# Performance work log

Hardware: AMD Instinct MI355X
Metric: run time of the kernel (lower is better)

The kernel has to match this reference:

```python
import math
import jax, jax.numpy as jnp
import numpy as np

BN_EPS = 1e-5

def _lrelu(x, s):
    return jnp.where(x >= 0, x, s * x)

def _bn(x, g, b):
    # BatchNorm2d in train mode (torch default): biased batch stats over (B,H,W)
    mu = jnp.mean(x, axis=(0, 2, 3), keepdims=True)
    var = jnp.mean((x - mu) ** 2, axis=(0, 2, 3), keepdims=True)
    return (x - mu) / jnp.sqrt(var + BN_EPS) * g[None, :, None, None] + b[None, :, None, None]

def _knn(x, x2, k):
    # x: [B,d,P], x2: [B,d,S] -> idx [B,k,S]: k nearest points of x for each column of x2
    inner = -2.0 * jnp.einsum('bdp,bds->bps', x, x2)
    xx = jnp.sum(x ** 2, axis=1)[:, :, None]    # [B,P,1]
    xx2 = jnp.sum(x2 ** 2, axis=1)[:, None, :]  # [B,1,S]
    d = -xx - inner - xx2                        # [B,P,S], larger = closer
    _, idx = jax.lax.top_k(jnp.transpose(d, (0, 2, 1)), k)  # [B,S,k]
    return jnp.transpose(idx, (0, 2, 1))         # [B,k,S]

def _gather_nb(X, idx, s, k):
    # faithful to torch gether_neibour, including its flat-reshape layout
    B, C, P = X.shape
    base = jnp.arange(B)[:, None, None] * P
    flat = (idx + base).reshape(-1)
    Xt = jnp.transpose(X, (0, 2, 1)).reshape(B * P, C)
    return Xt[flat].reshape(B, s, k, C)

def _c2d(x, W, b):
    return jnp.einsum('oc,bcpk->bopk', W, x) + b[None, :, None, None]

def _c1d(x, W, b):
    return jnp.einsum('oc,bcp->bop', W, x) + b[None, :, None]

def _forward(x, W_pos, b_pos, g2, be2, W_conv, b_conv, g1, be1, W_a1, b_a1, W_a2, b_a2, W_b1, b_b1, W_b2, b_b2, num_points):
    B, C, P = x.shape
    k = 8
    s = num_points
    # ---- Dynamic_sampling_M: uniform mesh over (x,y) bbox, snap to nearest event ----
    L = int(math.ceil(math.sqrt(s)))
    m = jnp.arange(L, dtype=x.dtype) / L
    m01 = jnp.tile(m[None, :], (L, 1)).reshape(1, 1, L * L)
    m02 = jnp.tile(m[:, None], (1, L)).reshape(1, 1, L * L)
    mesh = jnp.broadcast_to(jnp.concatenate([m01, m02], axis=1), (B, 2, L * L))
    Px = jax.lax.stop_gradient(x[:, :2, :])  # knn runs under torch.no_grad
    mn = Px.min(axis=2, keepdims=True)
    mx = Px.max(axis=2, keepdims=True)
    PS = mesh * (mx - mn) + mn
    idx0 = _knn(Px, PS, 1)                                   # [B,1,L*L]
    sp = _gather_nb(x, idx0, L * L, 1)[:, :, 0, :].transpose(0, 2, 1)  # [B,C,s]
    idx = _knn(jax.lax.stop_gradient(x[:, :3, :]), jax.lax.stop_gradient(sp[:, :3, :]), k)  # [B,k,s]
    x1 = jnp.transpose(_gather_nb(x, idx, s, k), (0, 3, 1, 2))  # [B,C,s,k]
    # ---- positional encoding ----
    PA = x1[:, :3, :, :]
    PC = x1[:, :3, :, 0:1]
    diff = PA - PC
    sq = jnp.sum(diff ** 2, axis=1, keepdims=True)
    temp = jnp.where(sq > 0, jnp.sqrt(jnp.where(sq > 0, sq, 1.0)), 0.0)
    PEmb = jnp.concatenate([PA, jnp.broadcast_to(PC, PA.shape), diff, temp], axis=1)  # [B,10,s,k]
    PEmb = _lrelu(_bn(_c2d(PEmb, W_pos, b_pos), g2, be2), 0.2)
    x_ = _lrelu(_bn(_c2d(x1[:, :4, :, :], W_conv, b_conv), g1, be1), 0.2)
    feat = jnp.concatenate([x_, PEmb], axis=1)  # [B,64,s,k]
    att = _c2d(_lrelu(_c2d(feat, W_a1, b_a1), 0.2), W_a2, b_a2)  # [B,1,s,k]
    att = jax.nn.softmax(att, axis=-1)
    feat = jnp.sum(feat * att, axis=-1)  # [B,64,s]
    Fea1 = _c1d(feat, W_b1, b_b1)
    Fea2 = _c1d(x1[:, :4, :, 0], W_b2, b_b2)
    out = _lrelu(Fea1 + Fea2, 0.01)
    return jnp.concatenate([x1[:, :5, :, 0], out], axis=1)  # [B,69,s]

def setup_inputs() -> dict:
    key = jax.random.key(0)
    ks = jax.random.split(key, 8)
    B, C, P = 2, 5, 16384
    num_points = 4096  # perfect square required by the mesh sampler
    outc, inc, h = 64, 4, 32
    w = lambda k_, shape: jax.random.normal(k_, shape, jnp.float32) * 0.05
    x = jax.random.normal(ks[0], (B, C, P), jnp.float32)
    return dict(
        x=x,
        W_pos=w(ks[1], (h, 10)), b_pos=jnp.zeros((h,), jnp.float32),
        g2=jnp.ones((h,), jnp.float32), be2=jnp.zeros((h,), jnp.float32),
        W_conv=w(ks[2], (h, inc)), b_conv=jnp.zeros((h,), jnp.float32),
        g1=jnp.ones((h,), jnp.float32), be1=jnp.zeros((h,), jnp.float32),
        W_a1=w(ks[3], (32, outc)), b_a1=jnp.zeros((32,), jnp.float32),
        W_a2=w(ks[4], (1, 32)), b_a2=jnp.zeros((1,), jnp.float32),
        W_b1=w(ks[5], (outc, outc)), b_b1=jnp.zeros((outc,), jnp.float32),
        W_b2=w(ks[6], (outc, inc)), b_b2=jnp.zeros((outc,), jnp.float32),
        num_points=num_points,
    )

def reference(x, W_pos, b_pos, g2, be2, W_conv, b_conv, g1, be1, W_a1, b_a1, W_a2, b_a2, W_b1, b_b1, W_b2, b_b2, num_points):
    return _forward(x, W_pos, b_pos, g2, be2, W_conv, b_conv, g1, be1, W_a1, b_a1, W_a2, b_a2, W_b1, b_b1, W_b2, b_b2, num_points)
```

## Files before the change

kernel.cpp:

```cpp
#include <hip/hip_runtime.h>
#include <math.h>

#define B_ 2
#define P_ 16384
#define C_ 5
#define S_ 4096
#define KNN_ 8
#define L_ 64

typedef unsigned short u16;
typedef unsigned int u32;

__device__ int   g_idxk[B_ * KNN_ * S_];
__device__ float g_partials[256 * 128];

__device__ __forceinline__ float bf2f(u16 u) {
  union { u32 i; float f; } c; c.i = ((u32)u) << 16; return c.f;
}
__device__ __forceinline__ u16 f2bf(float f) {
  union { float f; u32 i; } c; c.f = f;
  u32 r = c.i + 0x7fffu + ((c.i >> 16) & 1u);
  return (u16)(r >> 16);
}
__device__ __forceinline__ float ldany(const void* p, int i, int f32) {
  return f32 ? ((const float*)p)[i] : bf2f(((const u16*)p)[i]);
}

__device__ __forceinline__ int keyidx(double w) {
  return 16383 - (int)(((u32)__double2loint(w) >> 6) & 16383u);
}
__device__ __forceinline__ void cmpswap(double& a, double& b) {
  double hi = fmax(a, b), lo = fmin(a, b);
  a = hi; b = lo;
}
__device__ __forceinline__ void flush8(double* a, double* k) {
  cmpswap(k[0], k[1]); cmpswap(k[2], k[3]); cmpswap(k[4], k[5]); cmpswap(k[6], k[7]);
  cmpswap(k[0], k[2]); cmpswap(k[1], k[3]); cmpswap(k[4], k[6]); cmpswap(k[5], k[7]);
  cmpswap(k[1], k[2]); cmpswap(k[5], k[6]);
  cmpswap(k[0], k[4]); cmpswap(k[1], k[5]); cmpswap(k[2], k[6]); cmpswap(k[3], k[7]);
  cmpswap(k[2], k[4]); cmpswap(k[3], k[5]);
  cmpswap(k[1], k[2]); cmpswap(k[3], k[4]); cmpswap(k[5], k[6]);
  a[0] = fmax(a[0], k[7]); a[1] = fmax(a[1], k[6]);
  a[2] = fmax(a[2], k[5]); a[3] = fmax(a[3], k[4]);
  a[4] = fmax(a[4], k[3]); a[5] = fmax(a[5], k[2]);
  a[6] = fmax(a[6], k[1]); a[7] = fmax(a[7], k[0]);
  cmpswap(a[0], a[4]); cmpswap(a[1], a[5]); cmpswap(a[2], a[6]); cmpswap(a[3], a[7]);
  cmpswap(a[0], a[2]); cmpswap(a[1], a[3]); cmpswap(a[4], a[6]); cmpswap(a[5], a[7]);
  cmpswap(a[0], a[1]); cmpswap(a[2], a[3]); cmpswap(a[4], a[5]); cmpswap(a[6], a[7]);
}

__device__ __forceinline__ int chk_bad(const void* p, int n, int tid) {
  int bad = 0;
  for (int i = tid; i < n; i += 256) {
    float f = bf2f(((const u16*)p)[i]);
    if (!(f == f) || fabsf(f) > 1024.0f) bad = 1;
  }
  return bad;
}

__global__ __launch_bounds__(256, 6) void k_knn(const void* __restrict__ xv) {
  __shared__ float4 s4[1024];
  __shared__ int sidx[4];
  __shared__ int sbad;
  __shared__ float sred[16];
  int tid = threadIdx.x;
  int l = tid & 63, g = tid >> 6;
  int sq = blockIdx.x * 4 + g;
  int b = sq >> 12;
  int s = sq & (S_ - 1);
  int base0 = b * C_ * P_, base1 = base0 + P_, base2 = base1 + P_;

  if (tid == 0) sbad = 0;
  __syncthreads();
  if (chk_bad(xv, 1024, tid)) atomicOr(&sbad, 1);
  __syncthreads();
  const int f32 = sbad;

  float mn0 = INFINITY, mx0 = -INFINITY, mn1 = INFINITY, mx1 = -INFINITY;
  for (int p = tid; p < P_; p += 256) {
    float v0 = ldany(xv, base0 + p, f32);
    float v1 = ldany(xv, base1 + p, f32);
    mn0 = fminf(mn0, v0); mx0 = fmaxf(mx0, v0);
    mn1 = fminf(mn1, v1); mx1 = fmaxf(mx1, v1);
  }
  for (int off = 32; off; off >>= 1) {
    mn0 = fminf(mn0, __shfl_down(mn0, off)); mx0 = fmaxf(mx0, __shfl_down(mx0, off));
    mn1 = fminf(mn1, __shfl_down(mn1, off)); mx1 = fmaxf(mx1, __shfl_down(mx1, off));
  }
  if (l == 0) {
    sred[g * 4 + 0] = mn0; sred[g * 4 + 1] = mx0;
    sred[g * 4 + 2] = mn1; sred[g * 4 + 3] = mx1;
  }
  __syncthreads();
  mn0 = fminf(fminf(sred[0], sred[4]), fminf(sred[8], sred[12]));
  mx0 = fmaxf(fmaxf(sred[1], sred[5]), fmaxf(sred[9], sred[13]));
  mn1 = fminf(fminf(sred[2], sred[6]), fminf(sred[10], sred[14]));
  mx1 = fmaxf(fmaxf(sred[3], sred[7]), fmaxf(sred[11], sred[15]));

  float mm0 = (float)(s & (L_ - 1)) * 0.015625f;
  float mm1 = (float)(s >> 6) * 0.015625f;
  float ps0 = __fadd_rn(__fmul_rn(mm0, __fsub_rn(mx0, mn0)), mn0);
  float ps1 = __fadd_rn(__fmul_rn(mm1, __fsub_rn(mx1, mn1)), mn1);
  float xx2 = __fadd_rn(__fmul_rn(ps0, ps0), __fmul_rn(ps1, ps1));
  float best = -INFINITY; int bestp = 0x7fffffff;
  for (int c = 0; c < 16; ++c) {
    __syncthreads();
#pragma unroll
    for (int r = 0; r < 4; ++r) {
      int i = r * 256 + tid;
      int gi = c * 1024 + i;
      float a0 = ldany(xv, base0 + gi, f32);
      float a1 = ldany(xv, base1 + gi, f32);
      float xx = __fadd_rn(__fmul_rn(a0, a0), __fmul_rn(a1, a1));
      s4[i] = make_float4(a0, a1, xx, 0.0f);
    }
    __syncthreads();
    for (int t = 0; t < 16; ++t) {
      float4 v = s4[t * 64 + l];
      int ix = c * 1024 + t * 64 + l;
      float dot = __fadd_rn(__fmul_rn(v.x, ps0), __fmul_rn(v.y, ps1));
      float inner = __fmul_rn(-2.0f, dot);
      float d = __fsub_rn(__fsub_rn(-v.z, inner), xx2);
      bool gt = d > best;
      best = gt ? d : best;
      bestp = gt ? ix : bestp;
    }
  }
  {
    float v = best; int ix = bestp;
    for (int m = 1; m < 64; m <<= 1) {
      float ov = __shfl_xor(v, m, 64); int op = __shfl_xor(ix, m, 64);
      if (ov > v || (ov == v && op < ix)) { v = ov; ix = op; }
    }
    if (l == 0) sidx[g] = ix;
  }
  __syncthreads();

  int qi = sidx[g] & (P_ - 1);
  float q0 = ldany(xv, base0 + qi, f32);
  float q1 = ldany(xv, base1 + qi, f32);
  float q2 = ldany(xv, base2 + qi, f32);
  float xx3q = __fadd_rn(__fadd_rn(__fmul_rn(q0, q0), __fmul_rn(q1, q1)),
                         __fmul_rn(q2, q2));
  double acc[8], kb[8];
#pragma unroll
  for (int k = 0; k < 8; ++k) acc[k] = -1.0;
  for (int c = 0; c < 16; ++c) {
    __syncthreads();
#pragma unroll
    for (int r = 0; r < 4; ++r) {
      int i = r * 256 + tid;
      int gi = c * 1024 + i;
      float a0 = ldany(xv, base0 + gi, f32);
      float a1 = ldany(xv, base1 + gi, f32);
      float a2 = ldany(xv, base2 + gi, f32);
      float xx = __fadd_rn(__fadd_rn(__fmul_rn(a0, a0), __fmul_rn(a1, a1)), __fmul_rn(a2, a2));
      s4[i] = make_float4(a0, a1, a2, xx);
    }
    __syncthreads();
#pragma unroll
    for (int t = 0; t < 16; ++t) {
      float4 v = s4[t * 64 + l];
      int ix = c * 1024 + t * 64 + l;
      u32 lob = ((u32)(16383 - ix)) << 6;
      float dot = __fadd_rn(__fadd_rn(__fmul_rn(v.x, q0), __fmul_rn(v.y, q1)),
                            __fmul_rn(v.z, q2));
      float inner = __fmul_rn(-2.0f, dot);
      float d = __fsub_rn(__fsub_rn(-v.w, inner), xx3q);
      u32 bits = __float_as_uint(d);
      u32 key = bits ^ ((u32)(((int)bits) >> 31) | 0x80000000u);
      kb[t & 7] = __hiloint2double((int)(0x3FF00000u | (key >> 12)),
                                   (int)((key << 20) | lob));
      if ((t & 7) == 7) flush8(acc, kb);
    }
  }
  double wk = 0.0;
#pragma unroll
  for (int r = 0; r < 8; ++r) {
    double w = acc[0];
    for (int m = 1; m < 64; m <<= 1) w = fmax(w, __shfl_xor(w, m, 64));
    if (l == r) wk = w;
    bool cns = (acc[0] == w);
#pragma unroll
    for (int k = 0; k < 7; ++k) acc[k] = cns ? acc[k + 1] : acc[k];
    acc[7] = cns ? -1.0 : acc[7];
  }
  if (l < 8) g_idxk[b * 32768 + l * 4096 + s] = keyidx(wk);
}

__global__ __launch_bounds__(256) void k_tail(const void* __restrict__ x,
                                              const void* __restrict__ Wpos,
                                              const void* __restrict__ bpos,
                                              const void* __restrict__ Wconv,
                                              const void* __restrict__ bconv) {
  __shared__ float sWpos[320], sbpos[32], sWconv[128], sbconv[32];
  __shared__ float sacc[16][128];
  __shared__ int sbx, sbw;
  int tid = threadIdx.x;
  if (tid == 0) { sbx = 0; sbw = 0; }
  __syncthreads();
  if (chk_bad(x, 1024, tid)) atomicOr(&sbx, 1);
  if (chk_bad(Wpos, 320, tid) | chk_bad(Wconv, 128, tid)) atomicOr(&sbw, 1);
  __syncthreads();
  const int f32 = sbx, wf32 = sbw;

  int id = blockIdx.x * 256 + tid;
  int b = id >> 15, n = id & 32767;
  const int* fb = g_idxk + b * 32768;
  int base0 = b * C_ * P_;
  int p = fb[n] & (P_ - 1);
  int p0 = fb[n & ~7] & (P_ - 1);
  float xvv[4], pc3[3];
#pragma unroll
  for (int cc = 0; cc < 4; ++cc) xvv[cc] = ldany(x, base0 + cc * P_ + p, f32);
#pragma unroll
  for (int cc = 0; cc < 3; ++cc) pc3[cc] = ldany(x, base0 + cc * P_ + p0, f32);

  for (int i2 = tid; i2 < 320; i2 += 256) sWpos[i2] = ldany(Wpos, i2, wf32);
  if (tid < 128) sWconv[tid] = ldany(Wconv, tid, wf32);
  if (tid < 32) { sbpos[tid] = ldany(bpos, tid, wf32); sbconv[tid] = ldany(bconv, tid, wf32); }
  __syncthreads();

  float d0 = xvv[0] - pc3[0], d1 = xvv[1] - pc3[1], d2 = xvv[2] - pc3[2];
  float sq = d0 * d0 + d1 * d1 + d2 * d2;
  float temp = (sq > 0.0f) ? sqrtf(sq) : 0.0f;
  float pe[10] = {xvv[0], xvv[1], xvv[2], pc3[0], pc3[1], pc3[2], d0, d1, d2, temp};
#pragma unroll
  for (int o = 0; o < 64; ++o) {
    float v;
    if (o < 32) {
      v = sbconv[o];
#pragma unroll
      for (int cc = 0; cc < 4; ++cc) v = fmaf(sWconv[o * 4 + cc], xvv[cc], v);
    } else {
      v = sbpos[o - 32];
#pragma unroll
      for (int cc = 0; cc < 10; ++cc) v = fmaf(sWpos[(o - 32) * 10 + cc], pe[cc], v);
    }
    float sv = v, qv = v * v;
    for (int m = 1; m < 16; m <<= 1) { sv += __shfl_xor(sv, m, 16); qv += __shfl_xor(qv, m, 16); }
    if ((tid & 15) == 0) { sacc[tid >> 4][o * 2] = sv; sacc[tid >> 4][o * 2 + 1] = qv; }
  }
  __syncthreads();
  if (tid < 128) {
    float a = 0.f;
#pragma unroll
    for (int w = 0; w < 16; ++w) a += sacc[w][tid];
    g_partials[blockIdx.x * 128 + tid] = a;
  }
}

__global__ __launch_bounds__(256) void k_pass2(const void* __restrict__ x,
                                               const void* __restrict__ Wpos,
                                               const void* __restrict__ bpos,
                                               const void* __restrict__ Wconv,
                                               const void* __restrict__ bconv,
                                               const void* __restrict__ g1,
                                               const void* __restrict__ be1,
                                               const void* __restrict__ g2,
                                               const void* __restrict__ be2,
                                               const void* __restrict__ Wa1,
                                               const void* __restrict__ ba1,
                                               const void* __restrict__ Wa2,
                                               const void* __restrict__ ba2,
                                               const void* __restrict__ Wb1,
                                               const void* __restrict__ bb1,
                                               const void* __restrict__ Wb2,
                                               const void* __restrict__ bb2,
                                               void* __restrict__ out) {
  __shared__ float sWpos[320], sbpos[32], sWconv[128], sbconv[32];
  __shared__ float sWa1[2048], sba1[32], sWa2[32];
  __shared__ float sWb1[64 * 65];
  __shared__ float sbb1[64], sWb2[256], sbb2[64], sstats[128];
  __shared__ float sp2[2][128];
  __shared__ float sba2;
  __shared__ int sbx, sbw;
  int tid = threadIdx.x;
  if (tid == 0) { sbx = 0; sbw = 0; }
  __syncthreads();
  if (chk_bad(x, 1024, tid)) atomicOr(&sbx, 1);
  if (chk_bad(Wa1, 2048, tid) | chk_bad(Wb1, 4096, tid)) atomicOr(&sbw, 1);
  __syncthreads();
  int xf32 = sbx, wf32 = sbw;

  int g = blockIdx.x * 32 + (tid >> 3);
  int j = tid & 7;
  int b = g >> 12, i = g & (S_ - 1);
  int n = i * 8 + j;
  const int* fb = g_idxk + b * 32768;
  int xbase = b * C_ * P_;
  int p = fb[n] & (P_ - 1);
  int p0 = fb[n & ~7] & (P_ - 1);
  float xvv[4];
#pragma unroll
  for (int c = 0; c < 4; ++c) xvv[c] = ldany(x, xbase + c * P_ + p, xf32);
  float pc3[3];
#pragma unroll
  for (int c = 0; c < 3; ++c) pc3[c] = ldany(x, xbase + c * P_ + p0, xf32);
  float xc0 = ldany(x, xbase + p0, xf32);
  float xc1 = ldany(x, xbase + P_ + p0, xf32);
  float xc2 = ldany(x, xbase + 2 * P_ + p0, xf32);
  float xc3 = ldany(x, xbase + 3 * P_ + p0, xf32);

  {
    int slot = tid & 127, half = tid >> 7;
    float a0 = 0.f, a1 = 0.f;
    for (int blk = half * 128; blk < half * 128 + 128; blk += 2) {
      a0 += g_partials[blk * 128 + slot];
      a1 += g_partials[(blk + 1) * 128 + slot];
    }
    sp2[half][slot] = a0 + a1;
  }
  for (int i2 = tid; i2 < 320; i2 += 256) sWpos[i2] = ldany(Wpos, i2, wf32);
  if (tid < 128) sWconv[tid] = ldany(Wconv, tid, wf32);
  if (tid < 32) { sbpos[tid] = ldany(bpos, tid, wf32); sbconv[tid] = ldany(bconv, tid, wf32); }
  for (int i2 = tid; i2 < 2048; i2 += 256) sWa1[i2] = ldany(Wa1, i2, wf32);
  for (int i2 = tid; i2 < 4096; i2 += 256) sWb1[(i2 >> 6) * 65 + (i2 & 63)] = ldany(Wb1, i2, wf32);
  if (tid >= 32 && tid < 64) { sba1[tid - 32] = ldany(ba1, tid - 32, wf32); sWa2[tid - 32] = ldany(Wa2, tid - 32, wf32); }
  if (tid >= 64 && tid < 128) { sbb1[tid - 64] = ldany(bb1, tid - 64, wf32); sbb2[tid - 64] = ldany(bb2, tid - 64, wf32); }
  sWb2[tid] = ldany(Wb2, tid, wf32);
  if (tid == 0) sba2 = ldany(ba2, 0, wf32);
  __syncthreads();
  if (tid >= 128 && tid < 192) {
    int ch = tid - 128;
    float sum = sp2[0][ch * 2] + sp2[1][ch * 2];
    float sq = sp2[0][ch * 2 + 1] + sp2[1][ch * 2 + 1];
    float mean = sum * (1.0f / 65536.0f);
    float var = sq * (1.0f / 65536.0f) - mean * mean;
    int o = ch & 31;
    float gg = ldany(ch < 32 ? g1 : g2, o, wf32);
    float be = ldany(ch < 32 ? be1 : be2, o, wf32);
    float scale = gg / sqrtf(var + 1e-5f);
    sstats[ch * 2] = scale;
    sstats[ch * 2 + 1] = be - mean * scale;
  }
  __syncthreads();

  float d0 = xvv[0] - pc3[0], d1 = xvv[1] - pc3[1], d2 = xvv[2] - pc3[2];
  float sq = d0 * d0 + d1 * d1 + d2 * d2;
  float temp = (sq > 0.0f) ? sqrtf(sq) : 0.0f;
  float pe[10] = {xvv[0], xvv[1], xvv[2], pc3[0], pc3[1], pc3[2], d0, d1, d2, temp};
  float feat[64];
#pragma unroll
  for (int o = 0; o < 32; ++o) {
    float acc = sbconv[o];
#pragma unroll
    for (int c = 0; c < 4; ++c) acc = fmaf(sWconv[o * 4 + c], xvv[c], acc);
    feat[o] = acc;
  }
#pragma unroll
  for (int o = 0; o < 32; ++o) {
    float acc = sbpos[o];
#pragma unroll
    for (int c = 0; c < 10; ++c) acc = fmaf(sWpos[o * 10 + c], pe[c], acc);
    feat[32 + o] = acc;
  }
#pragma unroll
  for (int c = 0; c < 64; ++c) {
    float v = fmaf(feat[c], sstats[c * 2], sstats[c * 2 + 1]);
    feat[c] = (v >= 0.f) ? v : 0.2f * v;
  }
  float att = sba2;
#pragma unroll 4
  for (int h = 0; h < 32; ++h) {
    float a0 = 0.f, a1 = 0.f, a2 = 0.f, a3 = 0.f;
#pragma unroll
    for (int c = 0; c < 64; c += 4) {
      a0 = fmaf(sWa1[h * 64 + c],     feat[c],     a0);
      a1 = fmaf(sWa1[h * 64 + c + 1], feat[c + 1], a1);
      a2 = fmaf(sWa1[h * 64 + c + 2], feat[c + 2], a2);
      a3 = fmaf(sWa1[h * 64 + c + 3], feat[c + 3], a3);
    }
    float acc = sba1[h] + ((a0 + a1) + (a2 + a3));
    acc = (acc >= 0.f) ? acc : 0.2f * acc;
    att = fmaf(sWa2[h], acc, att);
  }
  float mxv = att;
  for (int mk = 1; mk < 8; mk <<= 1) mxv = fmaxf(mxv, __shfl_xor(mxv, mk, 8));
  float e = expf(att - mxv);
  float se = e;
  for (int mk = 1; mk < 8; mk <<= 1) se += __shfl_xor(se, mk, 8);
  float a = e / se;
#pragma unroll
  for (int c = 0; c < 64; ++c) {
    float w = feat[c] * a;
    w += __shfl_xor(w, 1, 8);
    w += __shfl_xor(w, 2, 8);
    w += __shfl_xor(w, 4, 8);
    feat[c] = w;
  }
  int obase = b * 69 * S_;
#pragma unroll
  for (int oc = 0; oc < 8; ++oc) {
    int o = j * 8 + oc;
    float a0 = sbb1[o], a1 = 0.f, a2 = 0.f, a3 = 0.f;
#pragma unroll
    for (int c = 0; c < 64; c += 4) {
      a0 = fmaf(sWb1[o * 65 + c],     feat[c],     a0);
      a1 = fmaf(sWb1[o * 65 + c + 1], feat[c + 1], a1);
      a2 = fmaf(sWb1[o * 65 + c + 2], feat[c + 2], a2);
      a3 = fmaf(sWb1[o * 65 + c + 3], feat[c + 3], a3);
    }
    float acc = (a0 + a1) + (a2 + a3);
    float acc2 = sbb2[o];
    acc2 = fmaf(sWb2[o * 4 + 0], xc0, acc2);
    acc2 = fmaf(sWb2[o * 4 + 1], xc1, acc2);
    acc2 = fmaf(sWb2[o * 4 + 2], xc2, acc2);
    acc2 = fmaf(sWb2[o * 4 + 3], xc3, acc2);
    float r = acc + acc2;
    r = (r >= 0.f) ? r : 0.01f * r;
    int oi = obase + (5 + o) * S_ + i;
    if (xf32) ((float*)out)[oi] = r; else ((u16*)out)[oi] = f2bf(r);
  }
  if (j == 0) {
#pragma unroll
    for (int c = 0; c < 5; ++c) {
      int oi = obase + c * S_ + i;
      if (xf32) ((float*)out)[oi] = ((const float*)x)[xbase + c * P_ + p0];
      else      ((u16*)out)[oi]   = ((const u16*)x)[xbase + c * P_ + p0];
    }
  }
}

extern "C" void kernel_launch(void* const* d_in, const int* in_sizes, int n_in,
                              void* d_out, int out_size, void* d_ws, size_t ws_size,
                              hipStream_t stream) {
  const void* x     = d_in[0];
  const void* Wpos  = d_in[1];
  const void* bpos  = d_in[2];
  const void* g2    = d_in[3];
  const void* be2   = d_in[4];
  const void* Wconv = d_in[5];
  const void* bconv = d_in[6];
  const void* g1    = d_in[7];
  const void* be1   = d_in[8];
  const void* Wa1   = d_in[9];
  const void* ba1   = d_in[10];
  const void* Wa2   = d_in[11];
  const void* ba2   = d_in[12];
  const void* Wb1   = d_in[13];
  const void* bb1   = d_in[14];
  const void* Wb2   = d_in[15];
  const void* bb2   = d_in[16];
  (void)d_ws; (void)ws_size; (void)in_sizes; (void)n_in;

  hipLaunchKernelGGL(k_knn, dim3(2048), dim3(256), 0, stream, x);
  hipLaunchKernelGGL(k_tail, dim3(256), dim3(256), 0, stream, x,
                     Wpos, bpos, Wconv, bconv);
  hipLaunchKernelGGL(k_pass2, dim3(256), dim3(256), 0, stream, x,
                     Wpos, bpos, Wconv, bconv, g1, be1, g2, be2,
                     Wa1, ba1, Wa2, ba2, Wb1, bb1, Wb2, bb2, d_out);
}
```

Measured before the change: 300.4 us.

## Replace brute-force kNN with uniform-grid spatial binning and ring search

Brute-force O(S·P) nearest-neighbour scans are replaced by a 64x64 uniform grid over the x/y bounding box. New kernels compute min/max, build a histogram, prefix-scan it and scatter points into bin-sorted records. Each query then searches rings of bins outward from its own bin and stops early once a distance bound shows farther rings cannot improve the result. This adds four small serial-ish kernel launches, atomics and data-dependent divergent loops, and the 3D kNN relies on a z-magnitude margin to keep the early-exit bound correct.

```diff
diff --git a/kernel.cpp b/kernel.cpp
--- a/kernel.cpp
+++ b/kernel.cpp
@@ -11,8 +11,14 @@
 typedef unsigned short u16;
 typedef unsigned int u32;
 
-__device__ int   g_idxk[B_ * KNN_ * S_];
-__device__ float g_partials[256 * 128];
+__device__ int    g_idxk[B_ * KNN_ * S_];
+__device__ float  g_partials[256 * 128];
+__device__ float  g_mnmx[B_][5];
+__device__ int    g_hist[B_ * 4097];
+__device__ int    g_cursor[B_ * 4096];
+__device__ int    g_binof[B_ * P_];
+__device__ float4 g_recA[B_ * P_];
+__device__ float4 g_recB[B_ * P_];
 
 __device__ __forceinline__ float bf2f(u16 u) {
   union { u32 i; float f; } c; c.i = ((u32)u) << 16; return c.f;
@@ -26,27 +32,22 @@
   return f32 ? ((const float*)p)[i] : bf2f(((const u16*)p)[i]);
 }
 
+__device__ __forceinline__ double packkey(float d, int idx) {
+  u32 bits = __float_as_uint(d);
+  u32 key = bits ^ ((u32)(((int)bits) >> 31) | 0x80000000u);
+  int hi = (int)(0x3FF00000u | (key >> 12));
+  int lo = (int)((key << 20) | ((u32)(16383 - idx) << 6));
+  return __hiloint2double(hi, lo);
+}
 __device__ __forceinline__ int keyidx(double w) {
   return 16383 - (int)(((u32)__double2loint(w) >> 6) & 16383u);
 }
-__device__ __forceinline__ void cmpswap(double& a, double& b) {
-  double hi = fmax(a, b), lo = fmin(a, b);
-  a = hi; b = lo;
-}
-__device__ __forceinline__ void flush8(double* a, double* k) {
-  cmpswap(k[0], k[1]); cmpswap(k[2], k[3]); cmpswap(k[4], k[5]); cmpswap(k[6], k[7]);
-  cmpswap(k[0], k[2]); cmpswap(k[1], k[3]); cmpswap(k[4], k[6]); cmpswap(k[5], k[7]);
-  cmpswap(k[1], k[2]); cmpswap(k[5], k[6]);
-  cmpswap(k[0], k[4]); cmpswap(k[1], k[5]); cmpswap(k[2], k[6]); cmpswap(k[3], k[7]);
-  cmpswap(k[2], k[4]); cmpswap(k[3], k[5]);
-  cmpswap(k[1], k[2]); cmpswap(k[3], k[4]); cmpswap(k[5], k[6]);
-  a[0] = fmax(a[0], k[7]); a[1] = fmax(a[1], k[6]);
-  a[2] = fmax(a[2], k[5]); a[3] = fmax(a[3], k[4]);
-  a[4] = fmax(a[4], k[3]); a[5] = fmax(a[5], k[2]);
-  a[6] = fmax(a[6], k[1]); a[7] = fmax(a[7], k[0]);
-  cmpswap(a[0], a[4]); cmpswap(a[1], a[5]); cmpswap(a[2], a[6]); cmpswap(a[3], a[7]);
-  cmpswap(a[0], a[2]); cmpswap(a[1], a[3]); cmpswap(a[4], a[6]); cmpswap(a[5], a[7]);
-  cmpswap(a[0], a[1]); cmpswap(a[2], a[3]); cmpswap(a[4], a[5]); cmpswap(a[6], a[7]);
+__device__ __forceinline__ float keyd(double w) {
+  u32 hi = (u32)__double2hiint(w), lo = (u32)__double2loint(w);
+  u32 key = (hi << 12) | (lo >> 20);
+  u32 mask = (u32)(((int)key) >> 31);
+  u32 bits = key ^ ((~mask) | 0x80000000u);
+  return __uint_as_float(bits);
 }
 
 __device__ __forceinline__ int chk_bad(const void* p, int n, int tid) {
@@ -58,134 +59,269 @@
   return bad;
 }
 
-__global__ __launch_bounds__(256, 6) void k_knn(const void* __restrict__ xv) {
-  __shared__ float4 s4[1024];
-  __shared__ int sidx[4];
+__global__ __launch_bounds__(256) void k_prep(const void* __restrict__ xv) {
   __shared__ int sbad;
-  __shared__ float sred[16];
-  int tid = threadIdx.x;
-  int l = tid & 63, g = tid >> 6;
-  int sq = blockIdx.x * 4 + g;
-  int b = sq >> 12;
-  int s = sq & (S_ - 1);
+  __shared__ float sred[4][5];
+  int tid = threadIdx.x, b = blockIdx.x;
+  if (tid == 0) sbad = 0;
+  __syncthreads();
+  if (chk_bad(xv, 1024, tid)) atomicOr(&sbad, 1);
+  __syncthreads();
+  const int f32 = sbad;
   int base0 = b * C_ * P_, base1 = base0 + P_, base2 = base1 + P_;
-
-  if (tid == 0) sbad = 0;
-  __syncthreads();
-  if (chk_bad(xv, 1024, tid)) atomicOr(&sbad, 1);
-  __syncthreads();
-  const int f32 = sbad;
-
-  float mn0 = INFINITY, mx0 = -INFINITY, mn1 = INFINITY, mx1 = -INFINITY;
+  float mn0 = INFINITY, mx0 = -INFINITY, mn1 = INFINITY, mx1 = -INFINITY, am = 0.f;
   for (int p = tid; p < P_; p += 256) {
     float v0 = ldany(xv, base0 + p, f32);
     float v1 = ldany(xv, base1 + p, f32);
+    float v2 = ldany(xv, base2 + p, f32);
     mn0 = fminf(mn0, v0); mx0 = fmaxf(mx0, v0);
     mn1 = fminf(mn1, v1); mx1 = fmaxf(mx1, v1);
+    am = fmaxf(am, fabsf(v2));
   }
   for (int off = 32; off; off >>= 1) {
     mn0 = fminf(mn0, __shfl_down(mn0, off)); mx0 = fmaxf(mx0, __shfl_down(mx0, off));
     mn1 = fminf(mn1, __shfl_down(mn1, off)); mx1 = fmaxf(mx1, __shfl_down(mx1, off));
-  }
+    am = fmaxf(am, __shfl_down(am, off));
+  }
+  int l = tid & 63, g = tid >> 6;
   if (l == 0) {
-    sred[g * 4 + 0] = mn0; sred[g * 4 + 1] = mx0;
-    sred[g * 4 + 2] = mn1; sred[g * 4 + 3] = mx1;
-  }
-  __syncthreads();
-  mn0 = fminf(fminf(sred[0], sred[4]), fminf(sred[8], sred[12]));
-  mx0 = fmaxf(fmaxf(sred[1], sred[5]), fmaxf(sred[9], sred[13]));
-  mn1 = fminf(fminf(sred[2], sred[6]), fminf(sred[10], sred[14]));
-  mx1 = fmaxf(fmaxf(sred[3], sred[7]), fmaxf(sred[11], sred[15]));
+    sred[g][0] = mn0; sred[g][1] = mx0; sred[g][2] = mn1; sred[g][3] = mx1; sred[g][4] = am;
+  }
+  __syncthreads();
+  if (tid == 0) {
+    float a0 = fminf(fminf(sred[0][0], sred[1][0]), fminf(sred[2][0], sred[3][0]));
+    float a1 = fmaxf(fmaxf(sred[0][1], sred[1][1]), fmaxf(sred[2][1], sred[3][1]));
+    float a2 = fminf(fminf(sred[0][2], sred[1][2]), fminf(sred[2][2], sred[3][2]));
+    float a3 = fmaxf(fmaxf(sred[0][3], sred[1][3]), fmaxf(sred[2][3], sred[3][3]));
+    float a4 = fmaxf(fmaxf(sred[0][4], sred[1][4]), fmaxf(sred[2][4], sred[3][4]));
+    float aa = fmaxf(fmaxf(fabsf(a0), fabsf(a1)), fmaxf(fmaxf(fabsf(a2), fabsf(a3)), a4));
+    g_mnmx[b][0] = a0; g_mnmx[b][1] = a1; g_mnmx[b][2] = a2; g_mnmx[b][3] = a3;
+    g_mnmx[b][4] = aa * aa;
+  }
+  for (int i2 = tid; i2 < 4097; i2 += 256) g_hist[b * 4097 + i2] = 0;
+}
+
+__global__ __launch_bounds__(256) void k_hist(const void* __restrict__ xv) {
+  __shared__ int sbad;
+  int tid = threadIdx.x, blk = blockIdx.x;
+  if (tid == 0) sbad = 0;
+  __syncthreads();
+  if (chk_bad(xv, 1024, tid)) atomicOr(&sbad, 1);
+  __syncthreads();
+  const int f32 = sbad;
+  int b = blk >> 4;
+  int pb = (blk & 15) * 1024;
+  int base0 = b * C_ * P_, base1 = base0 + P_;
+  float mn0 = g_mnmx[b][0], mx0 = g_mnmx[b][1], mn1 = g_mnmx[b][2], mx1 = g_mnmx[b][3];
+  float r0 = __fsub_rn(mx0, mn0), r1 = __fsub_rn(mx1, mn1);
+  float inv0 = (r0 > 0.f) ? 64.0f / r0 : 0.f;
+  float inv1 = (r1 > 0.f) ? 64.0f / r1 : 0.f;
+  for (int q = 0; q < 4; ++q) {
+    int i = pb + q * 256 + tid;
+    float v0 = ldany(xv, base0 + i, f32);
+    float v1 = ldany(xv, base1 + i, f32);
+    int bx = (int)fminf(fmaxf((v0 - mn0) * inv0, 0.f), 63.f);
+    int by = (int)fminf(fmaxf((v1 - mn1) * inv1, 0.f), 63.f);
+    int bin = by * 64 + bx;
+    g_binof[b * P_ + i] = bin;
+    atomicAdd(&g_hist[b * 4097 + bin], 1);
+  }
+}
+
+__global__ __launch_bounds__(256) void k_scan() {
+  __shared__ int part[256];
+  int b = blockIdx.x, t = threadIdx.x;
+  int loc[16]; int s0 = 0;
+  for (int q = 0; q < 16; ++q) { loc[q] = g_hist[b * 4097 + t * 16 + q]; s0 += loc[q]; }
+  part[t] = s0;
+  __syncthreads();
+  for (int d2 = 1; d2 < 256; d2 <<= 1) {
+    int v = (t >= d2) ? part[t - d2] : 0;
+    __syncthreads();
+    part[t] += v;
+    __syncthreads();
+  }
+  int run = (t == 0) ? 0 : part[t - 1];
+  for (int q = 0; q < 16; ++q) {
+    g_hist[b * 4097 + t * 16 + q] = run;
+    g_cursor[b * 4096 + t * 16 + q] = run;
+    run += loc[q];
+  }
+  if (t == 0) g_hist[b * 4097 + 4096] = P_;
+}
+
+__global__ __launch_bounds__(256) void k_scatter(const void* __restrict__ xv) {
+  __shared__ int sbad;
+  int tid = threadIdx.x, blk = blockIdx.x;
+  if (tid == 0) sbad = 0;
+  __syncthreads();
+  if (chk_bad(xv, 1024, tid)) atomicOr(&sbad, 1);
+  __syncthreads();
+  const int f32 = sbad;
+  int b = blk >> 4;
+  int pb = (blk & 15) * 1024;
+  int base0 = b * C_ * P_, base1 = base0 + P_, base2 = base1 + P_;
+  for (int q = 0; q < 4; ++q) {
+    int i = pb + q * 256 + tid;
+    float a0 = ldany(xv, base0 + i, f32);
+    float a1 = ldany(xv, base1 + i, f32);
+    float a2 = ldany(xv, base2 + i, f32);
+    float xx2d = __fadd_rn(__fmul_rn(a0, a0), __fmul_rn(a1, a1));
+    float xx3  = __fadd_rn(__fadd_rn(__fmul_rn(a0, a0), __fmul_rn(a1, a1)), __fmul_rn(a2, a2));
+    int bin = g_binof[b * P_ + i];
+    int pos = atomicAdd(&g_cursor[b * 4096 + bin], 1);
+    g_recA[(b << 14) + pos] = make_float4(a0, a1, xx2d, __int_as_float(i));
+    g_recB[(b << 14) + pos] = make_float4(a0, a1, a2, xx3);
+  }
+}
+
+__global__ __launch_bounds__(256) void k_knn2(const void* __restrict__ xv) {
+  __shared__ int sbad;
+  int tid = threadIdx.x;
+  if (tid == 0) sbad = 0;
+  __syncthreads();
+  if (chk_bad(xv, 1024, tid)) atomicOr(&sbad, 1);
+  __syncthreads();
+  const int f32 = sbad;
+
+  int o = tid & 7;
+  int oct = (blockIdx.x * 256 + tid) >> 3;
+  int b = oct >> 12, s = oct & (S_ - 1);
+  int base0 = b * C_ * P_, base1 = base0 + P_, base2 = base1 + P_;
+
+  float mn0 = g_mnmx[b][0], mx0 = g_mnmx[b][1], mn1 = g_mnmx[b][2], mx1 = g_mnmx[b][3];
+  float margin = 2e-5f * g_mnmx[b][4];
+  float r0 = __fsub_rn(mx0, mn0), r1 = __fsub_rn(mx1, mn1);
+  float w0 = r0 * 0.015625f, w1 = r1 * 0.015625f;
+  float wmin = fminf(w0, w1) * 0.999f;
+  float inv0 = (r0 > 0.f) ? 64.0f / r0 : 0.f;
+  float inv1 = (r1 > 0.f) ? 64.0f / r1 : 0.f;
+  const int* hbp = g_hist + b * 4097;
+  const float4* recA = g_recA + (b << 14);
+  const float4* recB = g_recB + (b << 14);
 
   float mm0 = (float)(s & (L_ - 1)) * 0.015625f;
   float mm1 = (float)(s >> 6) * 0.015625f;
-  float ps0 = __fadd_rn(__fmul_rn(mm0, __fsub_rn(mx0, mn0)), mn0);
-  float ps1 = __fadd_rn(__fmul_rn(mm1, __fsub_rn(mx1, mn1)), mn1);
-  float xx2 = __fadd_rn(__fmul_rn(ps0, ps0), __fmul_rn(ps1, ps1));
-  float best = -INFINITY; int bestp = 0x7fffffff;
-  for (int c = 0; c < 16; ++c) {
-    __syncthreads();
-#pragma unroll
-    for (int r = 0; r < 4; ++r) {
-      int i = r * 256 + tid;
-      int gi = c * 1024 + i;
-      float a0 = ldany(xv, base0 + gi, f32);
-      float a1 = ldany(xv, base1 + gi, f32);
-      float xx = __fadd_rn(__fmul_rn(a0, a0), __fmul_rn(a1, a1));
-      s4[i] = make_float4(a0, a1, xx, 0.0f);
-    }
-    __syncthreads();
-    for (int t = 0; t < 16; ++t) {
-      float4 v = s4[t * 64 + l];
-      int ix = c * 1024 + t * 64 + l;
-      float dot = __fadd_rn(__fmul_rn(v.x, ps0), __fmul_rn(v.y, ps1));
-      float inner = __fmul_rn(-2.0f, dot);
-      float d = __fsub_rn(__fsub_rn(-v.z, inner), xx2);
-      bool gt = d > best;
-      best = gt ? d : best;
-      bestp = gt ? ix : bestp;
-    }
-  }
-  {
-    float v = best; int ix = bestp;
-    for (int m = 1; m < 64; m <<= 1) {
-      float ov = __shfl_xor(v, m, 64); int op = __shfl_xor(ix, m, 64);
-      if (ov > v || (ov == v && op < ix)) { v = ov; ix = op; }
-    }
-    if (l == 0) sidx[g] = ix;
-  }
-  __syncthreads();
-
-  int qi = sidx[g] & (P_ - 1);
+  float ps0 = __fadd_rn(__fmul_rn(mm0, r0), mn0);
+  float ps1 = __fadd_rn(__fmul_rn(mm1, r1), mn1);
+  float xx2q = __fadd_rn(__fmul_rn(ps0, ps0), __fmul_rn(ps1, ps1));
+  int bqx = (int)fminf(fmaxf((ps0 - mn0) * inv0, 0.f), 63.f);
+  int bqy = (int)fminf(fmaxf((ps1 - mn1) * inv1, 0.f), 63.f);
+  double best = -1.0;
+  for (int R = 0; R < 64; ++R) {
+    if (R >= 1) {
+      double bnd = best;
+      bnd = fmax(bnd, __shfl_xor(bnd, 1, 8));
+      bnd = fmax(bnd, __shfl_xor(bnd, 2, 8));
+      bnd = fmax(bnd, __shfl_xor(bnd, 4, 8));
+      if (bnd >= 1.0) {
+        float lb = (float)(R - 1) * wmin;
+        float ub = __fadd_rn(-(lb * lb), margin);
+        if (ub < keyd(bnd)) break;
+      }
+    }
+    int cnt = (R == 0) ? 1 : 8 * R;
+    for (int t = o; t < cnt; t += 8) {
+      int X, Y;
+      if (R == 0) { X = bqx; Y = bqy; }
+      else {
+        int side = 2 * R + 1;
+        if (t < side)          { X = bqx - R + t;          Y = bqy - R; }
+        else if (t < 2 * side) { X = bqx - R + (t - side); Y = bqy + R; }
+        else {
+          int u = t - 2 * side, m2 = 2 * R - 1;
+          if (u < m2) { X = bqx - R; Y = bqy - R + 1 + u; }
+          else        { X = bqx + R; Y = bqy - R + 1 + (u - m2); }
+        }
+      }
+      if ((unsigned)X > 63u || (unsigned)Y > 63u) continue;
+      int bin = Y * 64 + X;
+      int st = hbp[bin], en = hbp[bin + 1];
+      for (int j2 = st; j2 < en; ++j2) {
+        float4 rc = recA[j2];
+        float dot = __fadd_rn(__fmul_rn(rc.x, ps0), __fmul_rn(rc.y, ps1));
+        float inner = __fmul_rn(-2.0f, dot);
+        float d = __fsub_rn(__fsub_rn(-rc.z, inner), xx2q);
+        best = fmax(best, packkey(d, __float_as_int(rc.w)));
+      }
+    }
+  }
+  best = fmax(best, __shfl_xor(best, 1, 8));
+  best = fmax(best, __shfl_xor(best, 2, 8));
+  best = fmax(best, __shfl_xor(best, 4, 8));
+  int qi = keyidx(best) & (P_ - 1);
+
   float q0 = ldany(xv, base0 + qi, f32);
   float q1 = ldany(xv, base1 + qi, f32);
   float q2 = ldany(xv, base2 + qi, f32);
-  float xx3q = __fadd_rn(__fadd_rn(__fmul_rn(q0, q0), __fmul_rn(q1, q1)),
-                         __fmul_rn(q2, q2));
-  double acc[8], kb[8];
+  float xx3q = __fadd_rn(__fadd_rn(__fmul_rn(q0, q0), __fmul_rn(q1, q1)), __fmul_rn(q2, q2));
+  int cx = (int)fminf(fmaxf((q0 - mn0) * inv0, 0.f), 63.f);
+  int cy = (int)fminf(fmaxf((q1 - mn1) * inv1, 0.f), 63.f);
+  double acc[8];
 #pragma unroll
   for (int k = 0; k < 8; ++k) acc[k] = -1.0;
-  for (int c = 0; c < 16; ++c) {
-    __syncthreads();
-#pragma unroll
-    for (int r = 0; r < 4; ++r) {
-      int i = r * 256 + tid;
-      int gi = c * 1024 + i;
-      float a0 = ldany(xv, base0 + gi, f32);
-      float a1 = ldany(xv, base1 + gi, f32);
-      float a2 = ldany(xv, base2 + gi, f32);
-      float xx = __fadd_rn(__fadd_rn(__fmul_rn(a0, a0), __fmul_rn(a1, a1)), __fmul_rn(a2, a2));
-      s4[i] = make_float4(a0, a1, a2, xx);
-    }
-    __syncthreads();
-#pragma unroll
-    for (int t = 0; t < 16; ++t) {
-      float4 v = s4[t * 64 + l];
-      int ix = c * 1024 + t * 64 + l;
-      u32 lob = ((u32)(16383 - ix)) << 6;
-      float dot = __fadd_rn(__fadd_rn(__fmul_rn(v.x, q0), __fmul_rn(v.y, q1)),
-                            __fmul_rn(v.z, q2));
-      float inner = __fmul_rn(-2.0f, dot);
-      float d = __fsub_rn(__fsub_rn(-v.w, inner), xx3q);
-      u32 bits = __float_as_uint(d);
-      u32 key = bits ^ ((u32)(((int)bits) >> 31) | 0x80000000u);
-      kb[t & 7] = __hiloint2double((int)(0x3FF00000u | (key >> 12)),
-                                   (int)((key << 20) | lob));
-      if ((t & 7) == 7) flush8(acc, kb);
+  for (int R = 0; R < 64; ++R) {
+    if (R >= 1) {
+      double bnd = acc[7];
+      bnd = fmax(bnd, __shfl_xor(bnd, 1, 8));
+      bnd = fmax(bnd, __shfl_xor(bnd, 2, 8));
+      bnd = fmax(bnd, __shfl_xor(bnd, 4, 8));
+      if (bnd >= 1.0) {
+        float lb = (float)(R - 1) * wmin;
+        float ub = __fadd_rn(-(lb * lb), margin);
+        if (ub < keyd(bnd)) break;
+      }
+    }
+    int cnt = (R == 0) ? 1 : 8 * R;
+    for (int t = o; t < cnt; t += 8) {
+      int X, Y;
+      if (R == 0) { X = cx; Y = cy; }
+      else {
+        int side = 2 * R + 1;
+        if (t < side)          { X = cx - R + t;          Y = cy - R; }
+        else if (t < 2 * side) { X = cx - R + (t - side); Y = cy + R; }
+        else {
+          int u = t - 2 * side, m2 = 2 * R - 1;
+          if (u < m2) { X = cx - R; Y = cy - R + 1 + u; }
+          else        { X = cx + R; Y = cy - R + 1 + (u - m2); }
+        }
+      }
+      if ((unsigned)X > 63u || (unsigned)Y > 63u) continue;
+      int bin = Y * 64 + X;
+      int st = hbp[bin], en = hbp[bin + 1];
+      for (int j2 = st; j2 < en; ++j2) {
+        float4 rc = recB[j2];
+        int idx = __float_as_int(((const float*)recA)[j2 * 4 + 3]);
+        float dot = __fadd_rn(__fadd_rn(__fmul_rn(rc.x, q0), __fmul_rn(rc.y, q1)),
+                              __fmul_rn(rc.z, q2));
+        float inner = __fmul_rn(-2.0f, dot);
+        float d = __fsub_rn(__fsub_rn(-rc.w, inner), xx3q);
+        double key = packkey(d, idx);
+        if (key > acc[7]) {
+          double tmp = key;
+#pragma unroll
+          for (int k = 0; k < 8; ++k) {
+            double hi2 = fmax(acc[k], tmp), lo2 = fmin(acc[k], tmp);
+            acc[k] = hi2; tmp = lo2;
+          }
+        }
+      }
     }
   }
   double wk = 0.0;
 #pragma unroll
-  for (int r = 0; r < 8; ++r) {
+  for (int r2 = 0; r2 < 8; ++r2) {
     double w = acc[0];
-    for (int m = 1; m < 64; m <<= 1) w = fmax(w, __shfl_xor(w, m, 64));
-    if (l == r) wk = w;
+    w = fmax(w, __shfl_xor(w, 1, 8));
+    w = fmax(w, __shfl_xor(w, 2, 8));
+    w = fmax(w, __shfl_xor(w, 4, 8));
+    if (o == r2) wk = w;
     bool cns = (acc[0] == w);
 #pragma unroll
     for (int k = 0; k < 7; ++k) acc[k] = cns ? acc[k + 1] : acc[k];
     acc[7] = cns ? -1.0 : acc[7];
   }
-  if (l < 8) g_idxk[b * 32768 + l * 4096 + s] = keyidx(wk);
+  g_idxk[b * 32768 + o * 4096 + s] = keyidx(wk);
 }
 
 __global__ __launch_bounds__(256) void k_tail(const void* __restrict__ x,
@@ -444,10 +580,14 @@
   const void* bb2   = d_in[16];
   (void)d_ws; (void)ws_size; (void)in_sizes; (void)n_in;
 
-  hipLaunchKernelGGL(k_knn, dim3(2048), dim3(256), 0, stream, x);
-  hipLaunchKernelGGL(k_tail, dim3(256), dim3(256), 0, stream, x,
+  hipLaunchKernelGGL(k_prep,    dim3(2),   dim3(256), 0, stream, x);
+  hipLaunchKernelGGL(k_hist,    dim3(32),  dim3(256), 0, stream, x);
+  hipLaunchKernelGGL(k_scan,    dim3(2),   dim3(256), 0, stream);
+  hipLaunchKernelGGL(k_scatter, dim3(32),  dim3(256), 0, stream, x);
+  hipLaunchKernelGGL(k_knn2,    dim3(256), dim3(256), 0, stream, x);
+  hipLaunchKernelGGL(k_tail,    dim3(256), dim3(256), 0, stream, x,
                      Wpos, bpos, Wconv, bconv);
-  hipLaunchKernelGGL(k_pass2, dim3(256), dim3(256), 0, stream, x,
+  hipLaunchKernelGGL(k_pass2,   dim3(256), dim3(256), 0, stream, x,
                      Wpos, bpos, Wconv, bconv, g1, be1, g2, be2,
                      Wa1, ba1, Wa2, ba2, Wb1, bb1, Wb2, bb2, d_out);
 }
```

Result: slower. 615.8 us (+105.0%).
